# Kernel optimization log

Hardware: AMD Instinct MI355X
Metric: run time of the kernel (lower is better)

## Reference

```python
import jax, jax.numpy as jnp
import numpy as np

B, N, C, H = 2, 2048, 1024, 16
D = C // H  # head_dim = 64


def setup_inputs() -> dict:
    key = jax.random.key(0)
    ks = jax.random.split(key, 5)
    s = 1.0 / np.sqrt(C)
    return {
        "q": jax.random.normal(ks[0], (B, N, C), dtype=jnp.float32),
        "W_qkv": jax.random.normal(ks[1], (C, 3 * C), dtype=jnp.float32) * s,
        "b_qkv": jnp.zeros((3 * C,), dtype=jnp.float32),
        "W_proj": jax.random.normal(ks[2], (C, C), dtype=jnp.float32) * s,
        "b_proj": jnp.zeros((C,), dtype=jnp.float32),
    }


def reference(q, W_qkv, b_qkv, W_proj, b_proj):
    # Self-attention: k = v = q. Full 3C projection (as in the torch code).
    qkv = q @ W_qkv + b_qkv  # [B, N, 3C]
    qh = qkv[:, :, :C].reshape(B, N, H, D)
    kh = qkv[:, :, C:2 * C].reshape(B, N, H, D)
    vh = qkv[:, :, 2 * C:].reshape(B, N, H, D)
    scale = D ** -0.5
    # [B, H, N, N] attention logits
    attn = jnp.einsum("bnhd,bmhd->bhnm", qh, kh) * scale
    attn = jax.nn.softmax(attn, axis=-1)
    out = jnp.einsum("bhnm,bmhd->bnhd", attn, vh).reshape(B, N, C)
    return out @ W_proj + b_proj
```

## Files before the change

### kernel.cpp

```cpp
#include <hip/hip_runtime.h>
#include <stdint.h>

typedef __bf16 bf16_t;
typedef __bf16 bf16x8 __attribute__((ext_vector_type(8)));
typedef __bf16 bf16x4 __attribute__((ext_vector_type(4)));
typedef float f32x4 __attribute__((ext_vector_type(4)));

#define L2E 1.44269504088896340736f
#define QSCALE (0.125f * L2E)

__device__ __forceinline__ void gload16(const bf16_t* g, bf16_t* l) {
  __builtin_amdgcn_global_load_lds(
      (const __attribute__((address_space(1))) void*)g,
      (__attribute__((address_space(3))) void*)l, 16, 0, 0);
}

__device__ __forceinline__ float fexp2(float x) {
  float r;
  asm("v_exp_f32 %0, %1" : "=v"(r) : "v"(x));
  return r;
}

__global__ __launch_bounds__(256) void prep_kernel(const float* __restrict__ qin,
                                                   bf16_t* __restrict__ qbf,
                                                   const float* __restrict__ wqkv,
                                                   bf16_t* __restrict__ wqkv_t,
                                                   const float* __restrict__ wproj,
                                                   bf16_t* __restrict__ wproj_t) {
  __shared__ float tile[64][65];
  const int bid = blockIdx.x, t = threadIdx.x;
  if (bid < 4096) {
    int i = bid * 256 + t;
    float4 v = reinterpret_cast<const float4*>(qin)[i];
    bf16x4 o;
    o[0] = (bf16_t)v.x; o[1] = (bf16_t)v.y; o[2] = (bf16_t)v.z; o[3] = (bf16_t)v.w;
    reinterpret_cast<bf16x4*>(qbf)[i] = o;
    return;
  }
  const float* in; bf16_t* out; int N, bx, by;
  if (bid < 4864) {
    int bb = bid - 4096; in = wqkv; out = wqkv_t; N = 3072; bx = bb % 48; by = bb / 48;
  } else {
    int bb = bid - 4864; in = wproj; out = wproj_t; N = 1024; bx = bb % 16; by = bb / 16;
  }
  const int K = 1024;
  int k0 = by * 64, n0 = bx * 64;
  int r = t >> 4, c4 = (t & 15) * 4;
#pragma unroll
  for (int rr = 0; rr < 4; rr++) {
    int row = r + rr * 16;
    float4 v = *reinterpret_cast<const float4*>(&in[(size_t)(k0 + row) * N + n0 + c4]);
    tile[row][c4 + 0] = v.x; tile[row][c4 + 1] = v.y;
    tile[row][c4 + 2] = v.z; tile[row][c4 + 3] = v.w;
  }
  __syncthreads();
#pragma unroll
  for (int rr = 0; rr < 4; rr++) {
    int nr = r + rr * 16;
    bf16x4 o;
#pragma unroll
    for (int i = 0; i < 4; i++) o[i] = (bf16_t)tile[c4 + i][nr];
    *reinterpret_cast<bf16x4*>(&out[(size_t)(n0 + nr) * K + k0 + c4]) = o;
  }
}

template <int MODE, int BM>
__global__ __launch_bounds__(256) void gemm_kernel(const bf16_t* __restrict__ A,
                                                   const bf16_t* __restrict__ Bt,
                                                   const float* __restrict__ bias,
                                                   void* __restrict__ out,
                                                   bf16_t* __restrict__ vT,
                                                   int K, int gm, int gn, int ldo) {
  constexpr int ACH = BM / 8;
  constexpr int NCH = ACH + 16;
  constexpr int CPW = NCH / 4;
  constexpr int IR = BM / 32;
  constexpr int SMEM = (MODE == 0) ? 17408 : (BM * 64 + 8192);
  __shared__ __align__(16) bf16_t smem[SMEM];
  bf16_t* At = smem;
  bf16_t* Bts = smem + BM * 64;
  const int t = threadIdx.x, lane = t & 63, w = t >> 6;
  const int g = lane >> 4, q = lane & 15;
  const int bid = blockIdx.x, x = bid & 7, r = bid >> 3;
  const int qm = gm >> 2, qn = gn >> 1;
  const int lm = r % qm, ln = r / qm;
  const int m0 = ((x & 3) * qm + lm) * BM, n0 = ((x >> 2) * qn + ln) * 128;
  const int wm = (w >> 1) * (BM / 2), wn = (w & 1) * 64;

  const bf16_t* srcp[CPW]; int dsto[CPW];
#pragma unroll
  for (int i = 0; i < CPW; i++) {
    int cI = i * 4 + w;
    bool isA = cI < ACH;
    int row = (isA ? cI : cI - ACH) * 8 + (lane >> 3);
    int p = (lane & 7) ^ (row & 7);
    srcp[i] = (isA ? A + (size_t)(m0 + row) * K : Bt + (size_t)(n0 + row) * K) + p * 8;
    dsto[i] = (isA ? cI * 512 : BM * 64 + (cI - ACH) * 512);
  }

  f32x4 acc[IR][4];
#pragma unroll
  for (int i = 0; i < IR; i++)
#pragma unroll
    for (int j = 0; j < 4; j++) acc[i][j] = (f32x4){0.f, 0.f, 0.f, 0.f};

  for (int k0 = 0; k0 < K; k0 += 64) {
    __syncthreads();
#pragma unroll
    for (int i = 0; i < CPW; i++) gload16(srcp[i] + k0, &smem[dsto[i]]);
    __syncthreads();
#pragma unroll
    for (int dc = 0; dc < 2; dc++) {
      bf16x8 am[IR], bn[4];
#pragma unroll
      for (int i = 0; i < IR; i++) {
        int ra = wm + 16 * i + q;
        am[i] = *reinterpret_cast<const bf16x8*>(&At[ra * 64 + ((dc * 32 + g * 8) ^ ((ra & 7) * 8))]);
      }
#pragma unroll
      for (int j = 0; j < 4; j++) {
        int rb = wn + 16 * j + q;
        bn[j] = *reinterpret_cast<const bf16x8*>(&Bts[rb * 64 + ((dc * 32 + g * 8) ^ ((rb & 7) * 8))]);
      }
#pragma unroll
      for (int i = 0; i < IR; i++)
#pragma unroll
        for (int j = 0; j < 4; j++)
          acc[i][j] = __builtin_amdgcn_mfma_f32_16x16x32_bf16(am[i], bn[j], acc[i][j], 0, 0, 0);
    }
  }

  if (MODE == 0 && n0 >= 2048) {
    __syncthreads();
    bf16_t* TT = smem;
#pragma unroll
    for (int i = 0; i < IR; i++)
#pragma unroll
      for (int j = 0; j < 4; j++)
#pragma unroll
        for (int rr = 0; rr < 4; rr++) {
          int ch = wn + 16 * j + q;
          int tok = wm + 16 * i + 4 * g + rr;
          float v = acc[i][j][rr] + bias[n0 + ch];
          TT[ch * 136 + (((tok >> 3) ^ (ch & 7)) * 8) + (tok & 7)] = (bf16_t)v;
        }
    __syncthreads();
    const int bb = m0 >> 11;
    const int t0 = m0 & 2047;
#pragma unroll
    for (int it = 0; it < 8; it++) {
      int ch = it * 16 + w * 4 + (lane >> 4);
      int ck = lane & 15;
      uint4 val = *reinterpret_cast<const uint4*>(&TT[ch * 136 + ((ck ^ (ch & 7)) * 8)]);
      int vch = (n0 - 2048) + ch;
      bf16_t* dst = vT + ((size_t)(bb * 16 + (vch >> 6)) * 64 + (vch & 63)) * 2048 + t0 + ck * 8;
      *reinterpret_cast<uint4*>(dst) = val;
    }
  } else {
#pragma unroll
    for (int i = 0; i < IR; i++)
#pragma unroll
      for (int j = 0; j < 4; j++)
#pragma unroll
        for (int rr = 0; rr < 4; rr++) {
          int row = m0 + wm + 16 * i + 4 * g + rr;
          int col = n0 + wn + 16 * j + q;
          float v = acc[i][j][rr] + bias[col];
          if (MODE == 0) {
            if (col < 1024) v *= QSCALE;
            ((bf16_t*)out)[(size_t)row * ldo + col] = (bf16_t)v;
          } else {
            ((float*)out)[(size_t)row * ldo + col] = v;
          }
        }
  }
}

__global__ __launch_bounds__(256) void attn_kernel(const bf16_t* __restrict__ qk,
                                                   const bf16_t* __restrict__ vT,
                                                   bf16_t* __restrict__ aout) {
  __shared__ __align__(16) bf16_t sK[2][4096];
  __shared__ __align__(16) bf16_t sV[2][4096];
  __shared__ __align__(16) bf16_t sP[4][1024];

  const int t = threadIdx.x, lane = t & 63, w = t >> 6;
  const int g = lane >> 4, q = lane & 15;
  const int bid = blockIdx.x, xr = bid >> 3;
  const int bh = (bid & 7) * 4 + (xr >> 5);
  const int b = bh >> 4, h = bh & 15;
  const int q0 = (xr & 31) * 64 + w * 16;
  const bf16_t* qk_b = qk + (size_t)b * 2048 * 2048;
  const bf16_t* vT_h = vT + (size_t)bh * 64 * 2048;
  bf16_t* Pw = sP[w];

  const bf16_t* srcK[2]; const bf16_t* srcV[2]; int dsto[2];
#pragma unroll
  for (int i = 0; i < 2; i++) {
    int gI = (w * 2 + i) * 64 + lane;
    int row = gI >> 3, p = (gI & 7) ^ (row & 7);
    srcK[i] = qk_b + (size_t)row * 2048 + 1024 + h * 64 + p * 8;
    srcV[i] = vT_h + (size_t)row * 2048 + p * 8;
    dsto[i] = (w * 2 + i) * 512;
  }

  bf16x8 bq[2];
  {
    const bf16_t* qr = qk_b + (size_t)(q0 + q) * 2048 + h * 64;
    bq[0] = *reinterpret_cast<const bf16x8*>(qr + g * 8);
    bq[1] = *reinterpret_cast<const bf16x8*>(qr + 32 + g * 8);
  }

  bf16x8 ones;
#pragma unroll
  for (int i = 0; i < 8; i++) ones[i] = (bf16_t)1.0f;

  f32x4 oacc[4];
#pragma unroll
  for (int c = 0; c < 4; c++) oacc[c] = (f32x4){0.f, 0.f, 0.f, 0.f};
  f32x4 lacc = (f32x4){0.f, 0.f, 0.f, 0.f};

#pragma unroll
  for (int i = 0; i < 2; i++) {
    gload16(srcK[i], &sK[0][dsto[i]]);
    gload16(srcV[i], &sV[0][dsto[i]]);
  }
  __syncthreads();

  for (int tt = 0; tt < 32; tt++) {
    const int cur = tt & 1;
    if (tt + 1 < 32) {
      size_t koffK = (size_t)(tt + 1) * 64 * 2048;
      size_t koffV = (size_t)(tt + 1) * 64;
#pragma unroll
      for (int i = 0; i < 2; i++) {
        gload16(srcK[i] + koffK, &sK[cur ^ 1][dsto[i]]);
        gload16(srcV[i] + koffV, &sV[cur ^ 1][dsto[i]]);
      }
    }

    const bf16_t* Kc = sK[cur];
    f32x4 s[4];
#pragma unroll
    for (int c = 0; c < 4; c++) {
      int row = 16 * c + q, sw = (q & 7) * 8;
      bf16x8 ka0 = *reinterpret_cast<const bf16x8*>(&Kc[row * 64 + ((g * 8) ^ sw)]);
      bf16x8 ka1 = *reinterpret_cast<const bf16x8*>(&Kc[row * 64 + ((32 + g * 8) ^ sw)]);
      f32x4 z = (f32x4){0.f, 0.f, 0.f, 0.f};
      z = __builtin_amdgcn_mfma_f32_16x16x32_bf16(ka0, bq[0], z, 0, 0, 0);
      z = __builtin_amdgcn_mfma_f32_16x16x32_bf16(ka1, bq[1], z, 0, 0, 0);
      s[c] = z;
    }

#pragma unroll
    for (int c = 0; c < 4; c++) {
      bf16x4 pk;
#pragma unroll
      for (int rr = 0; rr < 4; rr++) pk[rr] = (bf16_t)fexp2(s[c][rr]);
      *reinterpret_cast<bf16x4*>(
          &Pw[q * 64 + (((2 * c + (g >> 1)) ^ (q & 7)) * 8) + (g & 1) * 4]) = pk;
    }

    const bf16_t* Vc = sV[cur];
#pragma unroll
    for (int kc = 0; kc < 2; kc++) {
      bf16x8 pb = *reinterpret_cast<const bf16x8*>(
          &Pw[q * 64 + (((kc * 4 + g) ^ (q & 7)) * 8)]);
      lacc = __builtin_amdgcn_mfma_f32_16x16x32_bf16(ones, pb, lacc, 0, 0, 0);
#pragma unroll
      for (int c = 0; c < 4; c++) {
        int row = 16 * c + q;
        bf16x8 va = *reinterpret_cast<const bf16x8*>(
            &Vc[row * 64 + (((kc * 4 + g) ^ (q & 7)) * 8)]);
        oacc[c] = __builtin_amdgcn_mfma_f32_16x16x32_bf16(va, pb, oacc[c], 0, 0, 0);
      }
    }

    __syncthreads();
  }

  float inv = 1.0f / lacc[0];
  bf16_t* orow = aout + (size_t)(b * 2048 + q0 + q) * 1024 + h * 64;
#pragma unroll
  for (int c = 0; c < 4; c++) {
    bf16x4 ov;
#pragma unroll
    for (int rr = 0; rr < 4; rr++) ov[rr] = (bf16_t)(oacc[c][rr] * inv);
    *reinterpret_cast<bf16x4*>(orow + c * 16 + g * 4) = ov;
  }
}

extern "C" void kernel_launch(void* const* d_in, const int* in_sizes, int n_in,
                              void* d_out, int out_size, void* d_ws, size_t ws_size,
                              hipStream_t stream) {
  const float* q     = (const float*)d_in[0];
  const float* Wqkv  = (const float*)d_in[1];
  const float* bqkv  = (const float*)d_in[2];
  const float* Wproj = (const float*)d_in[3];
  const float* bproj = (const float*)d_in[4];
  float* out = (float*)d_out;

  char* ws = (char*)d_ws;
  bf16_t* q_bf    = (bf16_t*)(ws);
  bf16_t* wqkv_t  = (bf16_t*)(ws + 8388608);
  bf16_t* wproj_t = (bf16_t*)(ws + 14680064);
  bf16_t* qk      = (bf16_t*)(ws + 16777216);
  bf16_t* vT      = (bf16_t*)(ws + 33554432);
  bf16_t* aout    = q_bf;

  prep_kernel<<<5120, 256, 0, stream>>>(q, q_bf, Wqkv, wqkv_t, Wproj, wproj_t);
  gemm_kernel<0, 128><<<768, 256, 0, stream>>>(q_bf, wqkv_t, bqkv, qk, vT, 1024, 32, 24, 2048);
  attn_kernel<<<1024, 256, 0, stream>>>(qk, vT, aout);
  gemm_kernel<1, 64><<<512, 256, 0, stream>>>(aout, wproj_t, bproj, out, nullptr, 1024, 64, 8, 1024);
}
```

Measured before the change: 130.2 us.

## Keep softmax probabilities in registers via 16x16x16 MFMA, drop LDS P round-trip

The attention kernel now feeds the exponentiated scores straight from registers into 16x16x16 bf16 MFMAs as the A operand, instead of writing P to shared memory and reading it back for 16x16x32 MFMAs. The row-sum is accumulated in fp32 with vector adds and cross-lane shuffles, replacing the extra MFMA against a ones vector. This removes LDS writes and reads of P per tile and one MFMA per k-chunk. In exchange it issues twice as many narrower MFMAs and narrower V loads from LDS, and the output stores become scattered 2-byte writes instead of 8-byte vectors.

```diff
diff --git a/kernel.cpp b/kernel.cpp
--- a/kernel.cpp
+++ b/kernel.cpp
@@ -5,6 +5,7 @@
 typedef __bf16 bf16x8 __attribute__((ext_vector_type(8)));
 typedef __bf16 bf16x4 __attribute__((ext_vector_type(4)));
 typedef float f32x4 __attribute__((ext_vector_type(4)));
+typedef short short4v __attribute__((ext_vector_type(4)));
 
 #define L2E 1.44269504088896340736f
 #define QSCALE (0.125f * L2E)
@@ -20,6 +21,22 @@
   asm("v_exp_f32 %0, %1" : "=v"(r) : "v"(x));
   return r;
 }
+
+#if __has_builtin(__builtin_amdgcn_mfma_f32_16x16x16_bf16)
+#define HAVE_X16 1
+__device__ __forceinline__ f32x4 mfma16(bf16x4 a, bf16x4 b, f32x4 c) {
+  return __builtin_amdgcn_mfma_f32_16x16x16_bf16(a, b, c, 0, 0, 0);
+}
+#elif __has_builtin(__builtin_amdgcn_mfma_f32_16x16x16bf16_1k)
+#define HAVE_X16 1
+__device__ __forceinline__ f32x4 mfma16(bf16x4 a, bf16x4 b, f32x4 c) {
+  union { bf16x4 h; short4v s; } ua, ub;
+  ua.h = a; ub.h = b;
+  return __builtin_amdgcn_mfma_f32_16x16x16bf16_1k(ua.s, ub.s, c, 0, 0, 0);
+}
+#else
+#define HAVE_X16 0
+#endif
 
 __global__ __launch_bounds__(256) void prep_kernel(const float* __restrict__ qin,
                                                    bf16_t* __restrict__ qbf,
@@ -181,7 +198,9 @@
                                                    bf16_t* __restrict__ aout) {
   __shared__ __align__(16) bf16_t sK[2][4096];
   __shared__ __align__(16) bf16_t sV[2][4096];
+#if !HAVE_X16
   __shared__ __align__(16) bf16_t sP[4][1024];
+#endif
 
   const int t = threadIdx.x, lane = t & 63, w = t >> 6;
   const int g = lane >> 4, q = lane & 15;
@@ -191,7 +210,6 @@
   const int q0 = (xr & 31) * 64 + w * 16;
   const bf16_t* qk_b = qk + (size_t)b * 2048 * 2048;
   const bf16_t* vT_h = vT + (size_t)bh * 64 * 2048;
-  bf16_t* Pw = sP[w];
 
   const bf16_t* srcK[2]; const bf16_t* srcV[2]; int dsto[2];
 #pragma unroll
@@ -210,14 +228,18 @@
     bq[1] = *reinterpret_cast<const bf16x8*>(qr + 32 + g * 8);
   }
 
+  f32x4 oacc[4];
+#pragma unroll
+  for (int c = 0; c < 4; c++) oacc[c] = (f32x4){0.f, 0.f, 0.f, 0.f};
+#if HAVE_X16
+  f32x4 psum4 = (f32x4){0.f, 0.f, 0.f, 0.f};
+#else
+  bf16_t* Pw = sP[w];
   bf16x8 ones;
 #pragma unroll
   for (int i = 0; i < 8; i++) ones[i] = (bf16_t)1.0f;
-
-  f32x4 oacc[4];
-#pragma unroll
-  for (int c = 0; c < 4; c++) oacc[c] = (f32x4){0.f, 0.f, 0.f, 0.f};
   f32x4 lacc = (f32x4){0.f, 0.f, 0.f, 0.f};
+#endif
 
 #pragma unroll
   for (int i = 0; i < 2; i++) {
@@ -251,6 +273,29 @@
       s[c] = z;
     }
 
+    const bf16_t* Vc = sV[cur];
+#if HAVE_X16
+    bf16x4 pa[4];
+#pragma unroll
+    for (int c = 0; c < 4; c++) {
+      f32x4 e;
+#pragma unroll
+      for (int rr = 0; rr < 4; rr++) e[rr] = fexp2(s[c][rr]);
+      psum4 += e;
+#pragma unroll
+      for (int rr = 0; rr < 4; rr++) pa[c][rr] = (bf16_t)e[rr];
+    }
+    const int m7 = q & 7, gh = g >> 1, gl = (g & 1) * 4;
+#pragma unroll
+    for (int dblk = 0; dblk < 4; dblk++) {
+      const bf16_t* vrow = &Vc[(dblk * 16 + q) * 64];
+#pragma unroll
+      for (int c = 0; c < 4; c++) {
+        bf16x4 vb = *reinterpret_cast<const bf16x4*>(&vrow[(((2 * c + gh) ^ m7) * 8) + gl]);
+        oacc[dblk] = mfma16(pa[c], vb, oacc[dblk]);
+      }
+    }
+#else
 #pragma unroll
     for (int c = 0; c < 4; c++) {
       bf16x4 pk;
@@ -259,8 +304,6 @@
       *reinterpret_cast<bf16x4*>(
           &Pw[q * 64 + (((2 * c + (g >> 1)) ^ (q & 7)) * 8) + (g & 1) * 4]) = pk;
     }
-
-    const bf16_t* Vc = sV[cur];
 #pragma unroll
     for (int kc = 0; kc < 2; kc++) {
       bf16x8 pb = *reinterpret_cast<const bf16x8*>(
@@ -274,10 +317,25 @@
         oacc[c] = __builtin_amdgcn_mfma_f32_16x16x32_bf16(va, pb, oacc[c], 0, 0, 0);
       }
     }
-
-    __syncthreads();
-  }
-
+#endif
+
+    __syncthreads();
+  }
+
+#if HAVE_X16
+  float psum = psum4[0] + psum4[1] + psum4[2] + psum4[3];
+  psum += __shfl_xor(psum, 16);
+  psum += __shfl_xor(psum, 32);
+  float invr[4];
+#pragma unroll
+  for (int rr = 0; rr < 4; rr++) invr[rr] = 1.0f / __shfl(psum, 4 * g + rr, 64);
+  bf16_t* obase = aout + (size_t)(b * 2048 + q0) * 1024 + h * 64 + q;
+#pragma unroll
+  for (int dblk = 0; dblk < 4; dblk++)
+#pragma unroll
+    for (int rr = 0; rr < 4; rr++)
+      obase[(size_t)(4 * g + rr) * 1024 + dblk * 16] = (bf16_t)(oacc[dblk][rr] * invr[rr]);
+#else
   float inv = 1.0f / lacc[0];
   bf16_t* orow = aout + (size_t)(b * 2048 + q0 + q) * 1024 + h * 64;
 #pragma unroll
@@ -287,6 +345,7 @@
     for (int rr = 0; rr < 4; rr++) ov[rr] = (bf16_t)(oacc[c][rr] * inv);
     *reinterpret_cast<bf16x4*>(orow + c * 16 + g * 4) = ov;
   }
+#endif
 }
 
 extern "C" void kernel_launch(void* const* d_in, const int* in_sizes, int n_in,
```

Result: slower. 134.3 us (+3.1%).
